# Kernel tuning notes

Measured on AMD Instinct MI355X. Metric: run time of the kernel, lower is better.

Reference implementation:

```python
import jax, jax.numpy as jnp
import numpy as np

DIM = 1024          # hidden_size
HEADS = 16
KDIM = DIM // 2     # expand_k = 0.5
VDIM = DIM          # expand_v = 1.0
DK = KDIM // HEADS  # 32 head key dim
DV = VDIM // HEADS  # 64 head value dim
LOW = 16            # gate_low_rank_dim
NORMALIZER = 16.0   # gate_logit_normalizer
EPS = 1e-5
B, T = 2, 4096


def setup_inputs() -> dict:
    key = jax.random.key(0)
    ks = jax.random.split(key, 9)
    def lin(k, sh, fan_in):
        return jax.random.normal(k, sh, jnp.float32) * (fan_in ** -0.5)
    return {
        "x":    jax.random.normal(ks[0], (B, T, DIM), jnp.float32),
        "Wq":   lin(ks[1], (DIM, KDIM), DIM),
        "Wk":   lin(ks[2], (DIM, KDIM), DIM),
        "Wv":   lin(ks[3], (DIM, VDIM), DIM),
        "Wgk1": lin(ks[4], (DIM, LOW), DIM),   # low-rank gate proj (no bias)
        "Wgk2": lin(ks[5], (LOW, KDIM), LOW),  # low-rank gate proj (with bias)
        "bgk2": jnp.zeros((KDIM,), jnp.float32),
        "Wg":   lin(ks[6], (DIM, VDIM), DIM),  # output gate proj (no bias)
        "gnw":  jnp.ones((DV,), jnp.float32),  # per-head RMSNorm weight
        "Wo":   lin(ks[7], (VDIM, DIM), VDIM),
    }


def _gla_scan(q, k, v, gk):
    # q,k,gk: (B,T,H,DK)  v: (B,T,H,DV)
    # recurrent form of chunked GLA: h_t = exp(gk_t) (x) h_{t-1} + k_t (outer) v_t
    scale = DK ** -0.5
    def step(h, inp):
        qt, kt, vt, gt = inp                      # (B,H,DK)/(B,H,DV)
        h = h * jnp.exp(gt)[..., None] + kt[..., None] * vt[..., None, :]
        ot = jnp.einsum('bhk,bhkv->bhv', qt * scale, h)
        return h, ot
    h0 = jnp.zeros((q.shape[0], HEADS, DK, DV), q.dtype)
    xs = tuple(jnp.moveaxis(a, 1, 0) for a in (q, k, v, gk))  # time-major
    _, o = jax.lax.scan(step, h0, xs)
    return jnp.moveaxis(o, 0, 1)                  # (B,T,H,DV)


def reference(x, Wq, Wk, Wv, Wgk1, Wgk2, bgk2, Wg, gnw, Wo):
    Bx, Tx, _ = x.shape
    q = (x @ Wq).reshape(Bx, Tx, HEADS, DK)
    k = (x @ Wk).reshape(Bx, Tx, HEADS, DK)
    v = (x @ Wv).reshape(Bx, Tx, HEADS, DV)
    # data-dependent log-decay gate: logsigmoid(low-rank proj) / normalizer
    gk = jax.nn.log_sigmoid((x @ Wgk1) @ Wgk2 + bgk2)
    gk = gk.reshape(Bx, Tx, HEADS, DK) / NORMALIZER
    o = _gla_scan(q, k, v, gk)                    # (B,T,H,DV)
    # fused per-head RMSNorm + swish output gate
    g = (x @ Wg).reshape(Bx, Tx, HEADS, DV)
    o = o * jax.lax.rsqrt(jnp.mean(o * o, axis=-1, keepdims=True) + EPS) * gnw
    o = o * (g * jax.nn.sigmoid(g))
    return o.reshape(Bx, Tx, VDIM) @ Wo
```

## Files before the change

### kernel.cpp

```cpp
#include <hip/hip_runtime.h>

typedef unsigned short u16;
typedef unsigned int u32;
typedef __attribute__((ext_vector_type(8))) short short8;
typedef __attribute__((ext_vector_type(4))) float f32x4;

#define KD 512
#define HEADS 16
#define DK 32
#define DV 64
#define TT 4096
#define MROWS 8192
#define CHUNK 64
#define NCH 64
#define NBH 32
#define QSTR 3328
#define SCALE 0.17677669529663687f

__device__ __forceinline__ u16 f2bf(float f) {
    union { float f; unsigned int u; } x; x.f = f;
    unsigned int u = x.u;
    unsigned int r = (u + 0x7fffu + ((u >> 16) & 1u)) >> 16;
    return (u16)r;
}
__device__ __forceinline__ float bf2f(u16 s) {
    union { unsigned int u; float f; } x; x.u = ((unsigned int)s) << 16;
    return x.f;
}
__device__ __forceinline__ void gload16(const u16* g, u16* l) {
    __builtin_amdgcn_global_load_lds((const __attribute__((address_space(1))) u32*)g,
                                     (__attribute__((address_space(3))) u32*)l, 16, 0, 0);
}

__global__ __launch_bounds__(256) void prep_fused(const float* __restrict__ x,
                                                  u16* __restrict__ xb,
                                                  const float* __restrict__ Wq,
                                                  const float* __restrict__ Wk,
                                                  const float* __restrict__ Wv,
                                                  const float* __restrict__ Wg,
                                                  const float* __restrict__ W1,
                                                  const float* __restrict__ Wo,
                                                  u16* __restrict__ dst) {
    __shared__ float tile[32][33];
    int bid = blockIdx.x;
    if (bid < 8192) {
        int i = bid * 256 + threadIdx.x;
        const float4 v = ((const float4*)x)[i];
        ushort4 o;
        o.x = f2bf(v.x); o.y = f2bf(v.y); o.z = f2bf(v.z); o.w = f2bf(v.w);
        ((ushort4*)xb)[i] = o;
        return;
    }
    int w = bid - 8192;
    int n0 = (w % 136) * 32, k0 = (w / 136) * 32;
    int tx = threadIdx.x & 31, ty = threadIdx.x >> 5;
    int n = n0 + tx;
    const float* src; int sN, cc;
    if (n < 512)       { src = Wq; sN = 512;  cc = n; }
    else if (n < 1024) { src = Wk; sN = 512;  cc = n - 512; }
    else if (n < 2048) { src = Wv; sN = 1024; cc = n - 1024; }
    else if (n < 3072) { src = Wg; sN = 1024; cc = n - 2048; }
    else if (n < 3088) { src = W1; sN = 16;   cc = n - 3072; }
    else if (n < 3328) { src = nullptr; sN = 0; cc = 0; }
    else               { src = Wo; sN = 1024; cc = n - 3328; }
    for (int r = ty; r < 32; r += 8)
        tile[r][tx] = src ? src[(size_t)(k0 + r) * sN + cc] : 0.f;
    __syncthreads();
    for (int r = ty; r < 32; r += 8)
        dst[(size_t)(n0 + r) * 1024 + k0 + tx] = f2bf(tile[tx][r]);
}

#define BARM() do { asm volatile("" ::: "memory"); __builtin_amdgcn_s_barrier(); asm volatile("" ::: "memory"); } while (0)
#define VMW(n) asm volatile("s_waitcnt vmcnt(" #n ")" ::: "memory")

template<int OUTBF>
__global__ __launch_bounds__(512, 2) void gemm8(const u16* __restrict__ A,
                                                const u16* __restrict__ Bt,
                                                void* __restrict__ C,
                                                int M, int N, int K, int nbx) {
    __shared__ u16 SA[2][16384];
    __shared__ u16 SB[2][16384];
    int nwg = gridDim.x, bid = blockIdx.x, cpx = nwg >> 3;
    int wg = (bid & 7) * cpx + (bid >> 3);
    int bx = wg % nbx, by = wg / nbx;
    int brow = by << 8, bcol = bx << 8;
    int tid = threadIdx.x;
    int wv = tid >> 6, lane = tid & 63;
    int wm = wv >> 2, wn = wv & 3;
    int l15 = lane & 15, hi = lane >> 4;
    int rxor = l15 & 7;

    int srw = tid >> 3;
    int sg8 = ((tid & 7) ^ (srw & 7)) << 3;
    const u16* aBase = A + (size_t)(brow + srw) * K + sg8;
    const u16* bBase = Bt + (size_t)(bcol + ((tid >> 8) << 6) + (srw & 31)) * K + sg8;

#define STAGE_A(b, h, tt) do { \
        const u16* s_ = aBase + (size_t)(tt) * 64 + (size_t)(h) * 64 * K; \
        gload16(s_,                    &SA[b][(h) * 8192 + tid * 8]); \
        gload16(s_ + (size_t)128 * K,  &SA[b][(h) * 8192 + 4096 + tid * 8]); \
    } while (0)
#define STAGE_B(b, h, tt) do { \
        const u16* s_ = bBase + (size_t)(tt) * 64 + (size_t)(h) * 32 * K; \
        gload16(s_,                    &SB[b][(h) * 8192 + tid * 8]); \
        gload16(s_ + (size_t)128 * K,  &SB[b][(h) * 8192 + 4096 + tid * 8]); \
    } while (0)

    int aRow = (wm * 64 + l15) * 64;
    int bRow = (wn * 32 + l15) * 64;
    int cg0 = (hi ^ rxor) << 3;
    int cg1 = ((4 + hi) ^ rxor) << 3;

#define READ_A(dst, mh, b) do { \
        _Pragma("unroll") \
        for (int mil_ = 0; mil_ < 4; ++mil_) { \
            dst[mil_ * 2 + 0] = *(const short8*)&SA[b][(mh) * 8192 + mil_ * 1024 + aRow + cg0]; \
            dst[mil_ * 2 + 1] = *(const short8*)&SA[b][(mh) * 8192 + mil_ * 1024 + aRow + cg1]; \
        } } while (0)
#define READ_B(dst, nh, b) do { \
        _Pragma("unroll") \
        for (int nil_ = 0; nil_ < 2; ++nil_) { \
            dst[nil_ * 2 + 0] = *(const short8*)&SB[b][(nh) * 8192 + nil_ * 1024 + bRow + cg0]; \
            dst[nil_ * 2 + 1] = *(const short8*)&SB[b][(nh) * 8192 + nil_ * 1024 + bRow + cg1]; \
        } } while (0)

    f32x4 acc[8][4];
    #pragma unroll
    for (int mi = 0; mi < 8; ++mi)
        #pragma unroll
        for (int ni = 0; ni < 4; ++ni)
            acc[mi][ni] = (f32x4){0.f, 0.f, 0.f, 0.f};

#define MM(mb, nb, AF, BF) do { \
        __builtin_amdgcn_s_setprio(1); \
        _Pragma("unroll") \
        for (int ks_ = 0; ks_ < 2; ++ks_) \
        _Pragma("unroll") \
        for (int mil_ = 0; mil_ < 4; ++mil_) \
        _Pragma("unroll") \
        for (int nil_ = 0; nil_ < 2; ++nil_) \
            acc[(mb) + mil_][(nb) + nil_] = __builtin_amdgcn_mfma_f32_16x16x32_bf16( \
                AF[mil_ * 2 + ks_], BF[nil_ * 2 + ks_], acc[(mb) + mil_][(nb) + nil_], 0, 0, 0); \
        __builtin_amdgcn_s_setprio(0); \
    } while (0)

    int NK = K >> 6, NI = NK >> 1;
    STAGE_B(0, 0, 0); STAGE_A(0, 0, 0); STAGE_A(0, 1, 0); STAGE_B(0, 1, 0);
    STAGE_B(1, 0, 1); STAGE_A(1, 0, 1); STAGE_A(1, 1, 1);
    VMW(6);
    BARM();

    short8 alo[8], ahi[8], bb[4];
    for (int i = 0; i < NI; ++i) {
        int ta = 2 * i + 1; if (ta >= NK) ta = NK - 1;
        int tb = 2 * i + 2; if (tb >= NK) tb = NK - 1;
        int tc = 2 * i + 3; if (tc >= NK) tc = NK - 1;
        STAGE_B(1, 1, ta);
        READ_A(alo, 0, 0); READ_B(bb, 0, 0);
        BARM(); MM(0, 0, alo, bb); BARM();
        STAGE_B(0, 0, tb);
        READ_A(ahi, 1, 0);
        BARM(); MM(4, 0, ahi, bb); BARM();
        STAGE_A(0, 0, tb); STAGE_A(0, 1, tb);
        READ_B(bb, 1, 0);
        BARM(); MM(4, 2, ahi, bb); MM(0, 2, alo, bb);
        VMW(8);
        BARM();
        STAGE_B(0, 1, tb);
        READ_A(alo, 0, 1); READ_B(bb, 0, 1);
        BARM(); MM(0, 0, alo, bb); BARM();
        STAGE_B(1, 0, tc);
        READ_A(ahi, 1, 1);
        BARM(); MM(4, 0, ahi, bb);
        VMW(10);
        BARM();
        STAGE_A(1, 0, tc); STAGE_A(1, 1, tc);
        READ_B(bb, 1, 1);
        BARM(); MM(4, 2, ahi, bb); MM(0, 2, alo, bb);
        VMW(6);
        BARM();
    }

    VMW(0);
    BARM();
    if (OUTBF) {
        u16* slab = &SA[0][0] + wv * (16 * 72);
        int r0 = brow + wm * 128;
        int c0 = bcol + wn * 64;
        int row = lane >> 2, colb = (lane & 3) * 8;
        #pragma unroll
        for (int mi = 0; mi < 8; ++mi) {
            #pragma unroll
            for (int ni = 0; ni < 4; ++ni)
                #pragma unroll
                for (int rr = 0; rr < 4; ++rr)
                    slab[(hi * 4 + rr) * 72 + ni * 16 + l15] = f2bf(acc[mi][ni][rr]);
            #pragma unroll
            for (int v = 0; v < 2; ++v) {
                short8 val = *(const short8*)&slab[row * 72 + colb + v * 32];
                *(short8*)((u16*)C + (size_t)(r0 + mi * 16 + row) * N + c0 + colb + v * 32) = val;
            }
        }
    } else {
        int r0 = brow + wm * 128 + (hi << 2);
        int c0 = bcol + wn * 64 + l15;
        #pragma unroll
        for (int mi = 0; mi < 8; ++mi)
            #pragma unroll
            for (int ni = 0; ni < 4; ++ni)
                #pragma unroll
                for (int rr = 0; rr < 4; ++rr)
                    ((float*)C)[(size_t)(r0 + mi * 16 + rr) * N + (c0 + ni * 16)] = acc[mi][ni][rr];
    }
#undef STAGE_A
#undef STAGE_B
#undef READ_A
#undef READ_B
#undef MM
}

template<int OUTBF>
__global__ __launch_bounds__(256) void gemm_sb(const u16* __restrict__ A,
                                               const u16* __restrict__ Bt,
                                               void* __restrict__ C,
                                               int M, int N, int K, int nbx) {
    __shared__ u16 As[128 * 64];
    __shared__ u16 Bs[128 * 64];
    int nwg = gridDim.x;
    int bid = blockIdx.x;
    int cpx = nwg >> 3;
    int wg = (bid & 7) * cpx + (bid >> 3);
    int bx = wg % nbx, by = wg / nbx;
    int tid = threadIdx.x;
    int wave = tid >> 6, lane = tid & 63;
    int wr = wave >> 1, wc = wave & 1;
    int brow = by * 128, bcol = bx * 128;
    int srow = tid >> 3;
    int sgrp = (tid & 7) ^ (srow & 7);
    const u16* aS = A + (size_t)(brow + srow) * K + sgrp * 8;
    const u16* bS = Bt + (size_t)(bcol + srow) * K + sgrp * 8;
    f32x4 acc[4][4];
    #pragma unroll
    for (int mi = 0; mi < 4; ++mi)
        #pragma unroll
        for (int ni = 0; ni < 4; ++ni)
            acc[mi][ni] = (f32x4){0.f, 0.f, 0.f, 0.f};
    int l15 = lane & 15, hi = lane >> 4;
    int rxor = l15 & 7;
    for (int kt = 0; kt < K; kt += 64) {
        __syncthreads();
        #pragma unroll
        for (int i_ = 0; i_ < 4; ++i_) {
            gload16(aS + (size_t)i_ * 32 * K + kt, As + tid * 8 + i_ * 2048);
            gload16(bS + (size_t)i_ * 32 * K + kt, Bs + tid * 8 + i_ * 2048);
        }
        __syncthreads();
        #pragma unroll
        for (int ks = 0; ks < 2; ++ks) {
            short8 af[4], bfr[4];
            int g = ks * 4 + hi;
            #pragma unroll
            for (int i = 0; i < 4; ++i)
                af[i] = *(const short8*)(As + (size_t)(wr * 64 + i * 16 + l15) * 64 + ((g ^ rxor) << 3));
            #pragma unroll
            for (int i = 0; i < 4; ++i)
                bfr[i] = *(const short8*)(Bs + (size_t)(wc * 64 + i * 16 + l15) * 64 + ((g ^ rxor) << 3));
            #pragma unroll
            for (int mi = 0; mi < 4; ++mi)
                #pragma unroll
                for (int ni = 0; ni < 4; ++ni)
                    acc[mi][ni] = __builtin_amdgcn_mfma_f32_16x16x32_bf16(af[mi], bfr[ni], acc[mi][ni], 0, 0, 0);
        }
    }
    __syncthreads();
    if (!OUTBF) {
        float* slab = (float*)(wave < 2 ? (void*)As : (void*)Bs) + (wave & 1) * (16 * 68);
        int r0 = brow + wr * 64, c0 = bcol + wc * 64;
        int row = lane >> 2, colb = (lane & 3) * 4;
        #pragma unroll
        for (int mi = 0; mi < 4; ++mi) {
            #pragma unroll
            for (int ni = 0; ni < 4; ++ni)
                #pragma unroll
                for (int rr = 0; rr < 4; ++rr)
                    slab[(hi * 4 + rr) * 68 + ni * 16 + l15] = acc[mi][ni][rr];
            #pragma unroll
            for (int v = 0; v < 4; ++v) {
                float4 val = *(const float4*)&slab[row * 68 + colb + v * 16];
                *(float4*)((float*)C + (size_t)(r0 + mi * 16 + row) * N + c0 + colb + v * 16) = val;
            }
        }
    } else {
        u16* slab = As + wave * (16 * 72);
        int r0 = brow + wr * 64, c0 = bcol + wc * 64;
        int row = lane >> 2, colb = (lane & 3) * 8;
        #pragma unroll
        for (int mi = 0; mi < 4; ++mi) {
            #pragma unroll
            for (int ni = 0; ni < 4; ++ni)
                #pragma unroll
                for (int rr = 0; rr < 4; ++rr)
                    slab[(hi * 4 + rr) * 72 + ni * 16 + l15] = f2bf(acc[mi][ni][rr]);
            #pragma unroll
            for (int v = 0; v < 2; ++v) {
                short8 val = *(const short8*)&slab[row * 72 + colb + v * 32];
                *(short8*)((u16*)C + (size_t)(r0 + mi * 16 + row) * N + c0 + colb + v * 32) = val;
            }
        }
    }
}

__device__ __forceinline__ void gate_z8(const u16* __restrict__ xg,
                                        const float* __restrict__ W2,
                                        const float* __restrict__ b2,
                                        int cc, float* out8) {
    short8 x0 = *(const short8*)xg;
    short8 x1 = *(const short8*)(xg + 8);
    float z[8];
    float4 z0 = *(const float4*)(b2 + cc);
    float4 z1 = *(const float4*)(b2 + cc + 4);
    z[0]=z0.x; z[1]=z0.y; z[2]=z0.z; z[3]=z0.w;
    z[4]=z1.x; z[5]=z1.y; z[6]=z1.z; z[7]=z1.w;
    #pragma unroll
    for (int u = 0; u < 16; ++u) {
        float xu = bf2f((u16)(u < 8 ? x0[u] : x1[u - 8]));
        const float4 w0 = *(const float4*)(W2 + (size_t)u * 512 + cc);
        const float4 w1 = *(const float4*)(W2 + (size_t)u * 512 + cc + 4);
        z[0] += xu * w0.x; z[1] += xu * w0.y; z[2] += xu * w0.z; z[3] += xu * w0.w;
        z[4] += xu * w1.x; z[5] += xu * w1.y; z[6] += xu * w1.z; z[7] += xu * w1.w;
    }
    #pragma unroll
    for (int j = 0; j < 8; ++j) {
        float zz = z[j];
        out8[j] = (fminf(zz, 0.f) - log1pf(expf(-fabsf(zz)))) * 0.0625f;
    }
}

__device__ __forceinline__ void scan64(float (*gkS)[36], float* Ztot, int tid) {
    int wv2 = tid >> 6, ln = tid & 63;
    #pragma unroll
    for (int ii = 0; ii < 8; ++ii) {
        int i = wv2 * 8 + ii;
        float v = gkS[ln][i];
        #pragma unroll
        for (int d = 1; d < 64; d <<= 1) {
            float u = __shfl_up(v, d);
            if (ln >= d) v += u;
        }
        gkS[ln][i] = v;
        if (Ztot && ln == 63) Ztot[i] = v;
    }
}

__global__ __launch_bounds__(256) void phaseA(const u16* __restrict__ qkvg,
                                              const float* __restrict__ W2,
                                              const float* __restrict__ b2,
                                              u16* __restrict__ MT_ws,
                                              float* __restrict__ D_ws) {
    int bh = blockIdx.x >> 6, c = blockIdx.x & 63;
    int b = bh >> 4, h = bh & 15;
    int t0 = b * TT + c * CHUNK;
    __shared__ float gkS[64][36];
    __shared__ u16 kdT_bf[32 * 72];
    __shared__ u16 VT_bf[64 * 72];
    __shared__ float Z[32];
    int tid = threadIdx.x;
    int s = tid >> 2, i0 = (tid & 3) << 3;
    {
        float ls[8];
        gate_z8(qkvg + (size_t)(t0 + s) * QSTR + 3072, W2, b2, h * DK + i0, ls);
        #pragma unroll
        for (int jj = 0; jj < 8; ++jj) gkS[s][i0 + jj] = ls[jj];
    }
    short8 kv = *(const short8*)(qkvg + (size_t)(t0 + s) * QSTR + 512 + h * DK + i0);
    {
        int j0 = (tid & 3) << 4;
        short8 v0 = *(const short8*)(qkvg + (size_t)(t0 + s) * QSTR + 1024 + h * DV + j0);
        short8 v1 = *(const short8*)(qkvg + (size_t)(t0 + s) * QSTR + 1024 + h * DV + j0 + 8);
        #pragma unroll
        for (int jj = 0; jj < 8; ++jj) {
            VT_bf[(j0 + jj) * 72 + s] = (u16)v0[jj];
            VT_bf[(j0 + 8 + jj) * 72 + s] = (u16)v1[jj];
        }
    }
    __syncthreads();
    scan64(gkS, Z, tid);
    __syncthreads();
    #pragma unroll
    for (int jj = 0; jj < 8; ++jj)
        kdT_bf[(i0 + jj) * 72 + s] = f2bf(expf(Z[i0 + jj] - gkS[s][i0 + jj]) * bf2f((u16)kv[jj]));
    __syncthreads();
    int wave = tid >> 6, lane = tid & 63, l15 = lane & 15, hi = lane >> 4;
    int it = wave & 1, jp = wave >> 1;
    size_t base = ((size_t)(bh * NCH + c)) * 2048;
    #pragma unroll
    for (int jj2 = 0; jj2 < 2; ++jj2) {
        int jt = jp * 2 + jj2;
        f32x4 mc = (f32x4){0.f, 0.f, 0.f, 0.f};
        #pragma unroll
        for (int kc = 0; kc < 2; ++kc) {
            short8 ak = *(const short8*)&kdT_bf[(it * 16 + l15) * 72 + kc * 32 + hi * 8];
            short8 bv = *(const short8*)&VT_bf[(jt * 16 + l15) * 72 + kc * 32 + hi * 8];
            mc = __builtin_amdgcn_mfma_f32_16x16x32_bf16(ak, bv, mc, 0, 0, 0);
        }
        #pragma unroll
        for (int rr = 0; rr < 4; ++rr)
            MT_ws[base + (size_t)(jt * 16 + l15) * 32 + it * 16 + hi * 4 + rr] = f2bf(mc[rr]);
    }
    if (tid < 32) D_ws[(size_t)(bh * NCH + c) * 32 + tid] = expf(Z[tid]);
}

__global__ __launch_bounds__(256) void phaseB(const u16* __restrict__ MT_ws,
                                              const float* __restrict__ D_ws,
                                              u16* __restrict__ HT_ws) {
    int idx = (blockIdx.x * 256 + threadIdx.x) * 2;
    int bh = idx >> 11;
    int ji = idx & 2047;
    int i = ji & 31;
    float h0 = 0.f, h1 = 0.f;
    size_t base = (size_t)bh * NCH * 2048 + ji;
    const float* dp = D_ws + (size_t)bh * NCH * 32 + i;
    #pragma unroll 4
    for (int c = 0; c < NCH; ++c) {
        u32 hp = ((u32)f2bf(h0)) | (((u32)f2bf(h1)) << 16);
        *(u32*)(HT_ws + base + (size_t)c * 2048) = hp;
        float d0 = dp[c * 32], d1 = dp[c * 32 + 1];
        u32 mp = *(const u32*)(MT_ws + base + (size_t)c * 2048);
        h0 = h0 * d0 + bf2f((u16)(mp & 0xffff));
        h1 = h1 * d1 + bf2f((u16)(mp >> 16));
    }
}

__global__ __launch_bounds__(256) void phaseC(const u16* __restrict__ qkvg,
                                              const float* __restrict__ W2,
                                              const float* __restrict__ b2,
                                              const u16* __restrict__ HT_ws,
                                              const float* __restrict__ gnw,
                                              u16* __restrict__ o_n) {
    int bh = blockIdx.x >> 6, c = blockIdx.x & 63;
    int b = bh >> 4, h = bh & 15;
    int t0 = b * TT + c * CHUNK;
    __shared__ float gkS[64][36];
    __shared__ u16 qh_bf[64 * 40];
    __shared__ u16 kt_bf[64 * 40];
    __shared__ u16 VT_bf[64 * 72];
    __shared__ u16 Ht_bf[64 * 40];
    u16* P_bf = (u16*)&gkS[0][0];
    int tid = threadIdx.x;
    int s = tid >> 2, i0 = (tid & 3) << 3;
    {
        float ls[8];
        gate_z8(qkvg + (size_t)(t0 + s) * QSTR + 3072, W2, b2, h * DK + i0, ls);
        #pragma unroll
        for (int jj = 0; jj < 8; ++jj) gkS[s][i0 + jj] = ls[jj];
    }
    short8 qv = *(const short8*)(qkvg + (size_t)(t0 + s) * QSTR + h * DK + i0);
    short8 kv = *(const short8*)(qkvg + (size_t)(t0 + s) * QSTR + 512 + h * DK + i0);
    {
        int j0 = (tid & 3) << 4;
        short8 v0 = *(const short8*)(qkvg + (size_t)(t0 + s) * QSTR + 1024 + h * DV + j0);
        short8 v1 = *(const short8*)(qkvg + (size_t)(t0 + s) * QSTR + 1024 + h * DV + j0 + 8);
        #pragma unroll
        for (int jj = 0; jj < 8; ++jj) {
            VT_bf[(j0 + jj) * 72 + s] = (u16)v0[jj];
            VT_bf[(j0 + 8 + jj) * 72 + s] = (u16)v1[jj];
        }
    }
    {
        const u16* hp = HT_ws + ((size_t)(bh * NCH + c)) * 2048 + tid * 8;
        short8 hv = *(const short8*)hp;
        int j = tid >> 2, ii0 = (tid & 3) << 3;
        *(short8*)&Ht_bf[j * 40 + ii0] = hv;
    }
    __syncthreads();
    scan64(gkS, nullptr, tid);
    __syncthreads();
    #pragma unroll
    for (int jj = 0; jj < 8; ++jj) {
        float Sv = gkS[s][i0 + jj];
        qh_bf[s * 40 + i0 + jj] = f2bf(bf2f((u16)qv[jj]) * expf(Sv) * SCALE);
        kt_bf[s * 40 + i0 + jj] = f2bf(bf2f((u16)kv[jj]) * expf(fminf(-Sv, 80.f)));
    }
    __syncthreads();
    int wave = tid >> 6, lane = tid & 63, l15 = lane & 15, hi = lane >> 4;
    int w = wave;
    short8 aq = *(const short8*)&qh_bf[(w * 16 + l15) * 40 + hi * 8];
    #pragma unroll
    for (int sn = 0; sn < 4; ++sn) {
        f32x4 sc = (f32x4){0.f, 0.f, 0.f, 0.f};
        if (sn <= w) {
            short8 bk = *(const short8*)&kt_bf[(sn * 16 + l15) * 40 + hi * 8];
            sc = __builtin_amdgcn_mfma_f32_16x16x32_bf16(aq, bk, sc, 0, 0, 0);
        }
        #pragma unroll
        for (int rr = 0; rr < 4; ++rr) {
            float val = sc[rr];
            if (sn > w || (sn == w && l15 > hi * 4 + rr)) val = 0.f;
            P_bf[(w * 16 + hi * 4 + rr) * 72 + sn * 16 + l15] = f2bf(val);
        }
    }
    __syncthreads();
    f32x4 acc[4];
    #pragma unroll
    for (int jn = 0; jn < 4; ++jn) {
        f32x4 a = (f32x4){0.f, 0.f, 0.f, 0.f};
        short8 bhf = *(const short8*)&Ht_bf[(jn * 16 + l15) * 40 + hi * 8];
        acc[jn] = __builtin_amdgcn_mfma_f32_16x16x32_bf16(aq, bhf, a, 0, 0, 0);
    }
    int nkc = (w < 2) ? 1 : 2;
    for (int kc = 0; kc < nkc; ++kc) {
        short8 ap = *(const short8*)&P_bf[(w * 16 + l15) * 72 + kc * 32 + hi * 8];
        #pragma unroll
        for (int jn = 0; jn < 4; ++jn) {
            short8 bv = *(const short8*)&VT_bf[(jn * 16 + l15) * 72 + kc * 32 + hi * 8];
            acc[jn] = __builtin_amdgcn_mfma_f32_16x16x32_bf16(ap, bv, acc[jn], 0, 0, 0);
        }
    }
    #pragma unroll
    for (int rr = 0; rr < 4; ++rr) {
        float sum2 = 0.f;
        #pragma unroll
        for (int jn = 0; jn < 4; ++jn) sum2 += acc[jn][rr] * acc[jn][rr];
        sum2 += __shfl_xor(sum2, 1);
        sum2 += __shfl_xor(sum2, 2);
        sum2 += __shfl_xor(sum2, 4);
        sum2 += __shfl_xor(sum2, 8);
        float rms = rsqrtf(sum2 * (1.f / 64.f) + 1e-5f);
        int t = w * 16 + hi * 4 + rr;
        #pragma unroll
        for (int jn = 0; jn < 4; ++jn) {
            int j = jn * 16 + l15;
            float g = bf2f(qkvg[(size_t)(t0 + t) * QSTR + 2048 + h * DV + j]);
            float sw = g / (1.f + expf(-g));
            float o = acc[jn][rr] * rms * gnw[j] * sw;
            o_n[(size_t)(t0 + t) * 1024 + h * DV + j] = f2bf(o);
        }
    }
}

extern "C" void kernel_launch(void* const* d_in, const int* in_sizes, int n_in,
                              void* d_out, int out_size, void* d_ws, size_t ws_size,
                              hipStream_t stream) {
    const float* x    = (const float*)d_in[0];
    const float* Wq   = (const float*)d_in[1];
    const float* Wk   = (const float*)d_in[2];
    const float* Wv   = (const float*)d_in[3];
    const float* Wgk1 = (const float*)d_in[4];
    const float* Wgk2 = (const float*)d_in[5];
    const float* bgk2 = (const float*)d_in[6];
    const float* Wg   = (const float*)d_in[7];
    const float* gnw  = (const float*)d_in[8];
    const float* Wo   = (const float*)d_in[9];

    char* ws = (char*)d_ws;
    size_t off = 0;
    u16* xb      = (u16*)(ws + off); off += (size_t)MROWS * 1024 * 2;
    u16* Wall    = (u16*)(ws + off); off += (size_t)4352 * 1024 * 2;
    u16* qkvg    = (u16*)(ws + off); off += (size_t)MROWS * QSTR * 2;
    u16* MT_ws   = (u16*)(ws + off); off += (size_t)NBH * NCH * 2048 * 2;
    float* D_ws  = (float*)(ws + off); off += (size_t)NBH * NCH * 32 * 4;
    u16* HT_ws   = (u16*)(ws + off); off += (size_t)NBH * NCH * 2048 * 2;
    u16* o_n     = (u16*)(ws + off); off += (size_t)MROWS * 1024 * 2;
    u16* WcatT   = Wall;
    u16* WoT     = Wall + (size_t)3328 * 1024;

    prep_fused<<<8192 + 136 * 32, 256, 0, stream>>>(x, xb, Wq, Wk, Wv, Wg, Wgk1, Wo, Wall);
    gemm8<1><<<416, 512, 0, stream>>>(xb, WcatT, qkvg, MROWS, QSTR, 1024, 13);
    phaseA<<<NBH * NCH, 256, 0, stream>>>(qkvg, Wgk2, bgk2, MT_ws, D_ws);
    phaseB<<<128, 256, 0, stream>>>(MT_ws, D_ws, HT_ws);
    phaseC<<<NBH * NCH, 256, 0, stream>>>(qkvg, Wgk2, bgk2, HT_ws, gnw, o_n);
    gemm_sb<0><<<8 * 64, 256, 0, stream>>>(o_n, WoT, d_out, MROWS, 1024, 1024, 8);
}
```

Measured before the change: 173.5 us.

## Pre-swizzle weights into MFMA fragment layout and load B directly to registers

The prep kernel now writes the transposed bf16 weights in a fragment-major layout that matches the MFMA B operand. Both GEMMs then load B straight from global memory into registers instead of staging it through LDS. This removes the B tile from LDS, which frees shared memory and cuts LDS traffic and barriers. The QKV GEMM pipeline becomes a simpler double-buffered A-only loop, and the output GEMM gains software pipelining. The cost is that each wave reloads B from global or L2 with less reuse across the block, and the register-resident B buffers raise register pressure.

```diff
diff --git a/kernel.cpp b/kernel.cpp
--- a/kernel.cpp
+++ b/kernel.cpp
@@ -40,7 +40,8 @@
                                                   const float* __restrict__ Wg,
                                                   const float* __restrict__ W1,
                                                   const float* __restrict__ Wo,
-                                                  u16* __restrict__ dst) {
+                                                  u16* __restrict__ dstQ,
+                                                  u16* __restrict__ dstO) {
     __shared__ float tile[32][33];
     int bid = blockIdx.x;
     if (bid < 8192) {
@@ -66,8 +67,15 @@
     for (int r = ty; r < 32; r += 8)
         tile[r][tx] = src ? src[(size_t)(k0 + r) * sN + cc] : 0.f;
     __syncthreads();
-    for (int r = ty; r < 32; r += 8)
-        dst[(size_t)(n0 + r) * 1024 + k0 + tx] = f2bf(tile[tx][r]);
+    for (int r = ty; r < 32; r += 8) {
+        int nn = n0 + r, k = k0 + tx;
+        u16 val = f2bf(tile[tx][r]);
+        u16* base = dstQ;
+        if (nn >= 3328) { base = dstO; nn -= 3328; }
+        size_t addr = ((size_t)(nn >> 4) * 32 + (k >> 5)) * 512
+                    + (size_t)(((nn & 15) + ((k >> 3) & 3) * 16) << 3) + (k & 7);
+        base[addr] = val;
+    }
 }
 
 #define BARM() do { asm volatile("" ::: "memory"); __builtin_amdgcn_s_barrier(); asm volatile("" ::: "memory"); } while (0)
@@ -75,11 +83,10 @@
 
 template<int OUTBF>
 __global__ __launch_bounds__(512, 2) void gemm8(const u16* __restrict__ A,
-                                                const u16* __restrict__ Bt,
+                                                const u16* __restrict__ WF,
                                                 void* __restrict__ C,
                                                 int M, int N, int K, int nbx) {
     __shared__ u16 SA[2][16384];
-    __shared__ u16 SB[2][16384];
     int nwg = gridDim.x, bid = blockIdx.x, cpx = nwg >> 3;
     int wg = (bid & 7) * cpx + (bid >> 3);
     int bx = wg % nbx, by = wg / nbx;
@@ -89,39 +96,44 @@
     int wm = wv >> 2, wn = wv & 3;
     int l15 = lane & 15, hi = lane >> 4;
     int rxor = l15 & 7;
-
     int srw = tid >> 3;
     int sg8 = ((tid & 7) ^ (srw & 7)) << 3;
     const u16* aBase = A + (size_t)(brow + srw) * K + sg8;
-    const u16* bBase = Bt + (size_t)(bcol + ((tid >> 8) << 6) + (srw & 31)) * K + sg8;
-
-#define STAGE_A(b, h, tt) do { \
-        const u16* s_ = aBase + (size_t)(tt) * 64 + (size_t)(h) * 64 * K; \
-        gload16(s_,                    &SA[b][(h) * 8192 + tid * 8]); \
-        gload16(s_ + (size_t)128 * K,  &SA[b][(h) * 8192 + 4096 + tid * 8]); \
+    int KD32 = K >> 5;
+    const u16* wBase = WF + (size_t)((bcol >> 4) + wn * 4) * KD32 * 512 + lane * 8;
+    int aRow = (wm * 64 + l15) * 64;
+
+#define STAGE_A(b, tt) do { \
+        const u16* s_ = aBase + (size_t)(tt) * 64; \
+        gload16(s_,                   &SA[b][tid * 8]); \
+        gload16(s_ + (size_t)128 * K, &SA[b][4096 + tid * 8]); \
+        gload16(s_ + (size_t)64 * K,  &SA[b][8192 + tid * 8]); \
+        gload16(s_ + (size_t)192 * K, &SA[b][12288 + tid * 8]); \
     } while (0)
-#define STAGE_B(b, h, tt) do { \
-        const u16* s_ = bBase + (size_t)(tt) * 64 + (size_t)(h) * 32 * K; \
-        gload16(s_,                    &SB[b][(h) * 8192 + tid * 8]); \
-        gload16(s_ + (size_t)128 * K,  &SB[b][(h) * 8192 + 4096 + tid * 8]); \
+#define LOADB(dst, k32) do { \
+        _Pragma("unroll") \
+        for (int q_ = 0; q_ < 4; ++q_) \
+        _Pragma("unroll") \
+        for (int ks_ = 0; ks_ < 2; ++ks_) \
+            dst[q_ * 2 + ks_] = *(const short8*)(wBase + ((size_t)q_ * KD32 + (k32) + ks_) * 512); \
     } while (0)
-
-    int aRow = (wm * 64 + l15) * 64;
-    int bRow = (wn * 32 + l15) * 64;
-    int cg0 = (hi ^ rxor) << 3;
-    int cg1 = ((4 + hi) ^ rxor) << 3;
-
-#define READ_A(dst, mh, b) do { \
-        _Pragma("unroll") \
-        for (int mil_ = 0; mil_ < 4; ++mil_) { \
-            dst[mil_ * 2 + 0] = *(const short8*)&SA[b][(mh) * 8192 + mil_ * 1024 + aRow + cg0]; \
-            dst[mil_ * 2 + 1] = *(const short8*)&SA[b][(mh) * 8192 + mil_ * 1024 + aRow + cg1]; \
-        } } while (0)
-#define READ_B(dst, nh, b) do { \
-        _Pragma("unroll") \
-        for (int nil_ = 0; nil_ < 2; ++nil_) { \
-            dst[nil_ * 2 + 0] = *(const short8*)&SB[b][(nh) * 8192 + nil_ * 1024 + bRow + cg0]; \
-            dst[nil_ * 2 + 1] = *(const short8*)&SB[b][(nh) * 8192 + nil_ * 1024 + bRow + cg1]; \
+#define COMPUTE(b, BB) do { \
+        _Pragma("unroll") \
+        for (int ks_ = 0; ks_ < 2; ++ks_) { \
+            int cg_ = (((ks_ * 4) + hi) ^ rxor) << 3; \
+            short8 af_[8]; \
+            _Pragma("unroll") \
+            for (int mh_ = 0; mh_ < 2; ++mh_) \
+            _Pragma("unroll") \
+            for (int mil_ = 0; mil_ < 4; ++mil_) \
+                af_[mh_ * 4 + mil_] = *(const short8*)&SA[b][mh_ * 8192 + mil_ * 1024 + aRow + cg_]; \
+            __builtin_amdgcn_s_setprio(1); \
+            _Pragma("unroll") \
+            for (int m_ = 0; m_ < 8; ++m_) \
+            _Pragma("unroll") \
+            for (int ni_ = 0; ni_ < 4; ++ni_) \
+                acc[m_][ni_] = __builtin_amdgcn_mfma_f32_16x16x32_bf16(af_[m_], BB[ni_ * 2 + ks_], acc[m_][ni_], 0, 0, 0); \
+            __builtin_amdgcn_s_setprio(0); \
         } } while (0)
 
     f32x4 acc[8][4];
@@ -131,58 +143,29 @@
         for (int ni = 0; ni < 4; ++ni)
             acc[mi][ni] = (f32x4){0.f, 0.f, 0.f, 0.f};
 
-#define MM(mb, nb, AF, BF) do { \
-        __builtin_amdgcn_s_setprio(1); \
-        _Pragma("unroll") \
-        for (int ks_ = 0; ks_ < 2; ++ks_) \
-        _Pragma("unroll") \
-        for (int mil_ = 0; mil_ < 4; ++mil_) \
-        _Pragma("unroll") \
-        for (int nil_ = 0; nil_ < 2; ++nil_) \
-            acc[(mb) + mil_][(nb) + nil_] = __builtin_amdgcn_mfma_f32_16x16x32_bf16( \
-                AF[mil_ * 2 + ks_], BF[nil_ * 2 + ks_], acc[(mb) + mil_][(nb) + nil_], 0, 0, 0); \
-        __builtin_amdgcn_s_setprio(0); \
-    } while (0)
-
-    int NK = K >> 6, NI = NK >> 1;
-    STAGE_B(0, 0, 0); STAGE_A(0, 0, 0); STAGE_A(0, 1, 0); STAGE_B(0, 1, 0);
-    STAGE_B(1, 0, 1); STAGE_A(1, 0, 1); STAGE_A(1, 1, 1);
-    VMW(6);
-    BARM();
-
-    short8 alo[8], ahi[8], bb[4];
-    for (int i = 0; i < NI; ++i) {
-        int ta = 2 * i + 1; if (ta >= NK) ta = NK - 1;
-        int tb = 2 * i + 2; if (tb >= NK) tb = NK - 1;
-        int tc = 2 * i + 3; if (tc >= NK) tc = NK - 1;
-        STAGE_B(1, 1, ta);
-        READ_A(alo, 0, 0); READ_B(bb, 0, 0);
-        BARM(); MM(0, 0, alo, bb); BARM();
-        STAGE_B(0, 0, tb);
-        READ_A(ahi, 1, 0);
-        BARM(); MM(4, 0, ahi, bb); BARM();
-        STAGE_A(0, 0, tb); STAGE_A(0, 1, tb);
-        READ_B(bb, 1, 0);
-        BARM(); MM(4, 2, ahi, bb); MM(0, 2, alo, bb);
-        VMW(8);
-        BARM();
-        STAGE_B(0, 1, tb);
-        READ_A(alo, 0, 1); READ_B(bb, 0, 1);
-        BARM(); MM(0, 0, alo, bb); BARM();
-        STAGE_B(1, 0, tc);
-        READ_A(ahi, 1, 1);
-        BARM(); MM(4, 0, ahi, bb);
-        VMW(10);
-        BARM();
-        STAGE_A(1, 0, tc); STAGE_A(1, 1, tc);
-        READ_B(bb, 1, 1);
-        BARM(); MM(4, 2, ahi, bb); MM(0, 2, alo, bb);
-        VMW(6);
-        BARM();
-    }
-
-    VMW(0);
-    BARM();
+    short8 bbA[8], bbB[8];
+    int NK = K >> 6;
+    LOADB(bbA, 0);
+    STAGE_A(0, 0);
+    for (int t = 0; t < NK; t += 2) {
+        STAGE_A(1, t + 1);
+        LOADB(bbB, (t + 1) * 2);
+        VMW(12);
+        BARM();
+        COMPUTE(0, bbA);
+        BARM();
+        if (t + 2 < NK) {
+            STAGE_A(0, t + 2);
+            LOADB(bbA, (t + 2) * 2);
+            VMW(12);
+        } else {
+            VMW(0);
+        }
+        BARM();
+        COMPUTE(1, bbB);
+        BARM();
+    }
+
     if (OUTBF) {
         u16* slab = &SA[0][0] + wv * (16 * 72);
         int r0 = brow + wm * 128;
@@ -213,68 +196,91 @@
                     ((float*)C)[(size_t)(r0 + mi * 16 + rr) * N + (c0 + ni * 16)] = acc[mi][ni][rr];
     }
 #undef STAGE_A
-#undef STAGE_B
-#undef READ_A
-#undef READ_B
-#undef MM
-}
-
-template<int OUTBF>
-__global__ __launch_bounds__(256) void gemm_sb(const u16* __restrict__ A,
-                                               const u16* __restrict__ Bt,
-                                               void* __restrict__ C,
-                                               int M, int N, int K, int nbx) {
-    __shared__ u16 As[128 * 64];
-    __shared__ u16 Bs[128 * 64];
-    int nwg = gridDim.x;
-    int bid = blockIdx.x;
-    int cpx = nwg >> 3;
+#undef LOADB
+#undef COMPUTE
+}
+
+__global__ __launch_bounds__(256) void gemm_o(const u16* __restrict__ A,
+                                              const u16* __restrict__ WF,
+                                              float* __restrict__ C,
+                                              int M, int N, int K, int nbx) {
+    __shared__ u16 SA2[2][8192];
+    int nwg = gridDim.x, bid = blockIdx.x, cpx = nwg >> 3;
     int wg = (bid & 7) * cpx + (bid >> 3);
     int bx = wg % nbx, by = wg / nbx;
+    int brow = by * 128, bcol = bx * 128;
     int tid = threadIdx.x;
     int wave = tid >> 6, lane = tid & 63;
     int wr = wave >> 1, wc = wave & 1;
-    int brow = by * 128, bcol = bx * 128;
+    int l15 = lane & 15, hi = lane >> 4;
+    int rxor = l15 & 7;
     int srow = tid >> 3;
-    int sgrp = (tid & 7) ^ (srow & 7);
-    const u16* aS = A + (size_t)(brow + srow) * K + sgrp * 8;
-    const u16* bS = Bt + (size_t)(bcol + srow) * K + sgrp * 8;
+    int sgrp = ((tid & 7) ^ (srow & 7)) << 3;
+    const u16* aS = A + (size_t)(brow + srow) * K + sgrp;
+    int KD32 = K >> 5;
+    const u16* wBase = WF + (size_t)((bcol >> 4) + wc * 4) * KD32 * 512 + lane * 8;
+
+#define STAGE_A2(b, tt) do { \
+        _Pragma("unroll") \
+        for (int i_ = 0; i_ < 4; ++i_) \
+            gload16(aS + (size_t)i_ * 32 * K + (tt), &SA2[b][tid * 8 + i_ * 2048]); \
+    } while (0)
+#define LOADB2(dst, k32) do { \
+        _Pragma("unroll") \
+        for (int q_ = 0; q_ < 4; ++q_) \
+        _Pragma("unroll") \
+        for (int ks_ = 0; ks_ < 2; ++ks_) \
+            dst[q_ * 2 + ks_] = *(const short8*)(wBase + ((size_t)q_ * KD32 + (k32) + ks_) * 512); \
+    } while (0)
+#define COMPUTE2(b, BB) do { \
+        _Pragma("unroll") \
+        for (int ks_ = 0; ks_ < 2; ++ks_) { \
+            int cg_ = (((ks_ * 4) + hi) ^ rxor) << 3; \
+            short8 af_[4]; \
+            _Pragma("unroll") \
+            for (int mi_ = 0; mi_ < 4; ++mi_) \
+                af_[mi_] = *(const short8*)&SA2[b][(size_t)(wr * 64 + mi_ * 16 + l15) * 64 + cg_]; \
+            __builtin_amdgcn_s_setprio(1); \
+            _Pragma("unroll") \
+            for (int mi_ = 0; mi_ < 4; ++mi_) \
+            _Pragma("unroll") \
+            for (int ni_ = 0; ni_ < 4; ++ni_) \
+                acc[mi_][ni_] = __builtin_amdgcn_mfma_f32_16x16x32_bf16(af_[mi_], BB[ni_ * 2 + ks_], acc[mi_][ni_], 0, 0, 0); \
+            __builtin_amdgcn_s_setprio(0); \
+        } } while (0)
+
     f32x4 acc[4][4];
     #pragma unroll
     for (int mi = 0; mi < 4; ++mi)
         #pragma unroll
         for (int ni = 0; ni < 4; ++ni)
             acc[mi][ni] = (f32x4){0.f, 0.f, 0.f, 0.f};
-    int l15 = lane & 15, hi = lane >> 4;
-    int rxor = l15 & 7;
-    for (int kt = 0; kt < K; kt += 64) {
-        __syncthreads();
-        #pragma unroll
-        for (int i_ = 0; i_ < 4; ++i_) {
-            gload16(aS + (size_t)i_ * 32 * K + kt, As + tid * 8 + i_ * 2048);
-            gload16(bS + (size_t)i_ * 32 * K + kt, Bs + tid * 8 + i_ * 2048);
-        }
-        __syncthreads();
-        #pragma unroll
-        for (int ks = 0; ks < 2; ++ks) {
-            short8 af[4], bfr[4];
-            int g = ks * 4 + hi;
-            #pragma unroll
-            for (int i = 0; i < 4; ++i)
-                af[i] = *(const short8*)(As + (size_t)(wr * 64 + i * 16 + l15) * 64 + ((g ^ rxor) << 3));
-            #pragma unroll
-            for (int i = 0; i < 4; ++i)
-                bfr[i] = *(const short8*)(Bs + (size_t)(wc * 64 + i * 16 + l15) * 64 + ((g ^ rxor) << 3));
-            #pragma unroll
-            for (int mi = 0; mi < 4; ++mi)
-                #pragma unroll
-                for (int ni = 0; ni < 4; ++ni)
-                    acc[mi][ni] = __builtin_amdgcn_mfma_f32_16x16x32_bf16(af[mi], bfr[ni], acc[mi][ni], 0, 0, 0);
-        }
-    }
-    __syncthreads();
-    if (!OUTBF) {
-        float* slab = (float*)(wave < 2 ? (void*)As : (void*)Bs) + (wave & 1) * (16 * 68);
+
+    short8 bbA[8], bbB[8];
+    int NK = K >> 6;
+    LOADB2(bbA, 0);
+    STAGE_A2(0, 0);
+    for (int t = 0; t < NK; t += 2) {
+        STAGE_A2(1, (t + 1) * 64);
+        LOADB2(bbB, (t + 1) * 2);
+        VMW(12);
+        BARM();
+        COMPUTE2(0, bbA);
+        BARM();
+        if (t + 2 < NK) {
+            STAGE_A2(0, (t + 2) * 64);
+            LOADB2(bbA, (t + 2) * 2);
+            VMW(12);
+        } else {
+            VMW(0);
+        }
+        BARM();
+        COMPUTE2(1, bbB);
+        BARM();
+    }
+
+    {
+        float* slab = (float*)&SA2[0][0] + wave * 1088;
         int r0 = brow + wr * 64, c0 = bcol + wc * 64;
         int row = lane >> 2, colb = (lane & 3) * 4;
         #pragma unroll
@@ -287,27 +293,13 @@
             #pragma unroll
             for (int v = 0; v < 4; ++v) {
                 float4 val = *(const float4*)&slab[row * 68 + colb + v * 16];
-                *(float4*)((float*)C + (size_t)(r0 + mi * 16 + row) * N + c0 + colb + v * 16) = val;
+                *(float4*)(C + (size_t)(r0 + mi * 16 + row) * N + c0 + colb + v * 16) = val;
             }
         }
-    } else {
-        u16* slab = As + wave * (16 * 72);
-        int r0 = brow + wr * 64, c0 = bcol + wc * 64;
-        int row = lane >> 2, colb = (lane & 3) * 8;
-        #pragma unroll
-        for (int mi = 0; mi < 4; ++mi) {
-            #pragma unroll
-            for (int ni = 0; ni < 4; ++ni)
-                #pragma unroll
-                for (int rr = 0; rr < 4; ++rr)
-                    slab[(hi * 4 + rr) * 72 + ni * 16 + l15] = f2bf(acc[mi][ni][rr]);
-            #pragma unroll
-            for (int v = 0; v < 2; ++v) {
-                short8 val = *(const short8*)&slab[row * 72 + colb + v * 32];
-                *(short8*)((u16*)C + (size_t)(r0 + mi * 16 + row) * N + c0 + colb + v * 32) = val;
-            }
-        }
-    }
+    }
+#undef STAGE_A2
+#undef LOADB2
+#undef COMPUTE2
 }
 
 __device__ __forceinline__ void gate_z8(const u16* __restrict__ xg,
@@ -555,19 +547,18 @@
     char* ws = (char*)d_ws;
     size_t off = 0;
     u16* xb      = (u16*)(ws + off); off += (size_t)MROWS * 1024 * 2;
-    u16* Wall    = (u16*)(ws + off); off += (size_t)4352 * 1024 * 2;
+    u16* WfragQ  = (u16*)(ws + off); off += (size_t)208 * 32 * 512 * 2;
+    u16* WfragO  = (u16*)(ws + off); off += (size_t)64 * 32 * 512 * 2;
     u16* qkvg    = (u16*)(ws + off); off += (size_t)MROWS * QSTR * 2;
     u16* MT_ws   = (u16*)(ws + off); off += (size_t)NBH * NCH * 2048 * 2;
     float* D_ws  = (float*)(ws + off); off += (size_t)NBH * NCH * 32 * 4;
     u16* HT_ws   = (u16*)(ws + off); off += (size_t)NBH * NCH * 2048 * 2;
     u16* o_n     = (u16*)(ws + off); off += (size_t)MROWS * 1024 * 2;
-    u16* WcatT   = Wall;
-    u16* WoT     = Wall + (size_t)3328 * 1024;
-
-    prep_fused<<<8192 + 136 * 32, 256, 0, stream>>>(x, xb, Wq, Wk, Wv, Wg, Wgk1, Wo, Wall);
-    gemm8<1><<<416, 512, 0, stream>>>(xb, WcatT, qkvg, MROWS, QSTR, 1024, 13);
+
+    prep_fused<<<8192 + 136 * 32, 256, 0, stream>>>(x, xb, Wq, Wk, Wv, Wg, Wgk1, Wo, WfragQ, WfragO);
+    gemm8<1><<<416, 512, 0, stream>>>(xb, WfragQ, qkvg, MROWS, QSTR, 1024, 13);
     phaseA<<<NBH * NCH, 256, 0, stream>>>(qkvg, Wgk2, bgk2, MT_ws, D_ws);
     phaseB<<<128, 256, 0, stream>>>(MT_ws, D_ws, HT_ws);
     phaseC<<<NBH * NCH, 256, 0, stream>>>(qkvg, Wgk2, bgk2, HT_ws, gnw, o_n);
-    gemm_sb<0><<<8 * 64, 256, 0, stream>>>(o_n, WoT, d_out, MROWS, 1024, 1024, 8);
-}
+    gemm_o<<<8 * 64, 256, 0, stream>>>(o_n, WfragO, (float*)d_out, MROWS, 1024, 1024, 8);
+}
```

Result: slower. 292.5 us (+68.6%).
